# Kernel optimization log

Hardware: AMD Instinct MI355X
Metric: run time of the kernel (lower is better)

Reference implementation:

```python
import jax, jax.numpy as jnp
from jax import lax
import numpy as np

DIM = 384
NUM_HEADS = 8
HEAD_DIM = DIM // NUM_HEADS


def setup_inputs() -> dict:
    key = jax.random.key(0)
    k_x, k_qw, k_qb, k_lw, k_lb = jax.random.split(key, 5)
    B, H, W = 2, 64, 64
    N = H * W
    x = jax.random.normal(k_x, (B, N, DIM), dtype=jnp.float32)
    # nn.Linear(dim, 3*dim): weight (3C, C), bias (3C,)
    qkv_w = jax.random.normal(k_qw, (3 * DIM, DIM), dtype=jnp.float32) * (1.0 / np.sqrt(DIM))
    qkv_b = jax.random.normal(k_qb, (3 * DIM,), dtype=jnp.float32) * 0.02
    # nn.Conv2d(dim, dim, 3, padding=1, groups=dim): weight (C, 1, 3, 3), bias (C,)
    lepe_w = jax.random.normal(k_lw, (DIM, 1, 3, 3), dtype=jnp.float32) * (1.0 / 3.0)
    lepe_b = jax.random.normal(k_lb, (DIM,), dtype=jnp.float32) * 0.02
    return {"x": x, "qkv_w": qkv_w, "qkv_b": qkv_b, "lepe_w": lepe_w, "lepe_b": lepe_b, "H": H, "W": W}


def reference(x, qkv_w, qkv_b, lepe_w, lepe_b, H, W):
    B, N, C = x.shape
    hd = C // NUM_HEADS
    scale = hd ** -0.5
    # qkv projection: (B, N, 3C) -> (B, N, 3, heads, head_dim)
    qkv = (jnp.einsum('bnc,oc->bno', x, qkv_w) + qkv_b).reshape(B, N, 3, NUM_HEADS, hd)
    q, k, v = qkv[:, :, 0], qkv[:, :, 1], qkv[:, :, 2]  # each (B, N, heads, hd)
    attn = jnp.einsum('bnhd,bmhd->bhnm', q * scale, k)   # (B, heads, N, N)
    attn = jax.nn.softmax(attn, axis=-1)
    out = jnp.einsum('bhnm,bmhd->bnhd', attn, v).reshape(B, N, C)
    # LePE: depthwise 3x3 conv on v in NCHW layout
    v_img = v.reshape(B, H, W, C).transpose(0, 3, 1, 2)  # (B, C, H, W)
    lepe = lax.conv_general_dilated(
        v_img, lepe_w, window_strides=(1, 1), padding='SAME',
        feature_group_count=C,
        dimension_numbers=('NCHW', 'OIHW', 'NCHW'))
    lepe = lepe + lepe_b[None, :, None, None]
    return out + lepe.transpose(0, 2, 3, 1).reshape(B, N, C)
```

## Files before the change

kernel.cpp:

```cpp
#include <hip/hip_runtime.h>
#include <stdint.h>

#define DIM   384
#define NH    8
#define HD    48
#define HDP   64
#define NTOK  4096
#define KDIM  384
#define SCALE 0.14433756729740643f

typedef float  f32x4   __attribute__((ext_vector_type(4)));
typedef float  f32x16  __attribute__((ext_vector_type(16)));
typedef __bf16 bf16x8  __attribute__((ext_vector_type(8)));

__device__ __forceinline__ unsigned short f2bf(float f) {
  union { float f; unsigned int u; } c; c.f = f;
  unsigned int r = (c.u + 0x7FFFu + ((c.u >> 16) & 1u)) >> 16;
  return (unsigned short)r;
}
__device__ __forceinline__ float bf2f(unsigned short h) {
  union { unsigned int u; float f; } c; c.u = ((unsigned int)h) << 16;
  return c.f;
}


__global__ void prep_kernel(const float* __restrict__ x, const float* __restrict__ w,
                            unsigned short* __restrict__ x_bf,
                            unsigned short* __restrict__ w_bf) {
  int tid = blockIdx.x * blockDim.x + threadIdx.x;
  int stride = gridDim.x * blockDim.x;
  for (int i = tid; i < 786432; i += stride) {
    float4 v = ((const float4*)x)[i];
    ushort4 o;
    o.x = f2bf(v.x); o.y = f2bf(v.y); o.z = f2bf(v.z); o.w = f2bf(v.w);
    ((ushort4*)x_bf)[i] = o;
  }
  for (int i = tid; i < 110592; i += stride) {
    float4 v = ((const float4*)w)[i];
    ushort4 o;
    o.x = f2bf(v.x); o.y = f2bf(v.y); o.z = f2bf(v.z); o.w = f2bf(v.w);
    ((ushort4*)w_bf)[i] = o;
  }
}

__global__ __launch_bounds__(256) void qkv_gemm(
    const unsigned short* __restrict__ A,
    const unsigned short* __restrict__ Bw,
    const float* __restrict__ bias,
    unsigned short* __restrict__ q_pad,
    unsigned short* __restrict__ k_pad,
    unsigned short* __restrict__ v_t) {
  __shared__ unsigned short ldsA[128 * 32];
  __shared__ unsigned short ldsB[64 * 32];
  const int tid = threadIdx.x;
  const int wv = tid >> 6, ln = tid & 63;
  const int lrow = ln & 15, lq = ln >> 4;
  const int m0 = blockIdx.x * 128;
  const int n0 = blockIdx.y * 64;
  const int wm = (wv >> 1) * 64, wn = (wv & 1) * 32;

  f32x4 acc[4][2];
#pragma unroll
  for (int mi = 0; mi < 4; ++mi)
#pragma unroll
    for (int ni = 0; ni < 2; ++ni)
#pragma unroll
      for (int r = 0; r < 4; ++r) acc[mi][ni][r] = 0.f;

  for (int k0 = 0; k0 < KDIM; k0 += 32) {
    __syncthreads();
#pragma unroll
    for (int j = 0; j < 2; ++j) {
      int r16 = wv * 2 + j;
      const unsigned short* ga = A + (size_t)(m0 + r16 * 16 + (ln >> 2)) * KDIM
                                   + k0 + (ln & 3) * 8;
      __builtin_amdgcn_global_load_lds(
          (const __attribute__((address_space(1))) void*)ga,
          (__attribute__((address_space(3))) void*)&ldsA[r16 * 512], 16, 0, 0);
    }
    const unsigned short* gb = Bw + (size_t)(n0 + wv * 16 + (ln >> 2)) * KDIM
                                  + k0 + (ln & 3) * 8;
    __builtin_amdgcn_global_load_lds(
        (const __attribute__((address_space(1))) void*)gb,
        (__attribute__((address_space(3))) void*)&ldsB[wv * 512], 16, 0, 0);
    __syncthreads();
    bf16x8 af[4], bfv[2];
#pragma unroll
    for (int mi = 0; mi < 4; ++mi)
      af[mi] = *(const bf16x8*)&ldsA[(wm + mi * 16 + lrow) * 32 + lq * 8];
#pragma unroll
    for (int ni = 0; ni < 2; ++ni)
      bfv[ni] = *(const bf16x8*)&ldsB[(wn + ni * 16 + lrow) * 32 + lq * 8];
#pragma unroll
    for (int mi = 0; mi < 4; ++mi)
#pragma unroll
      for (int ni = 0; ni < 2; ++ni)
        acc[mi][ni] = __builtin_amdgcn_mfma_f32_16x16x32_bf16(
            af[mi], bfv[ni], acc[mi][ni], 0, 0, 0);
  }

#pragma unroll
  for (int mi = 0; mi < 4; ++mi)
#pragma unroll
    for (int ni = 0; ni < 2; ++ni)
#pragma unroll
      for (int r = 0; r < 4; ++r) {
        int row = m0 + wm + mi * 16 + lq * 4 + r;
        int col = n0 + wn + ni * 16 + lrow;
        float val = acc[mi][ni][r] + bias[col];
        int b = row >> 12;
        int n = row & 4095;
        if (col < 384) {
          int h = col / 48, d = col - h * 48;
          q_pad[((size_t)(b * 8 + h) * NTOK + n) * HDP + d] = f2bf(val * SCALE);
        } else if (col < 768) {
          int o = col - 384;
          int h = o / 48, d = o - h * 48;
          k_pad[((size_t)(b * 8 + h) * NTOK + n) * HDP + d] = f2bf(val);
        } else {
          int o = col - 768;
          v_t[((size_t)b * DIM + o) * NTOK + n] = f2bf(val);
        }
      }
}

__global__ __launch_bounds__(256) void lepe_kernel(
    const unsigned short* __restrict__ v_t,
    const float* __restrict__ lw, const float* __restrict__ lb,
    float* __restrict__ out) {
  __shared__ __align__(16) unsigned short pl[16 * 648];
  const int cg = blockIdx.x;
  const int sy = blockIdx.y;
  const int b  = blockIdx.z;
  const int t = threadIdx.x;
  const int y0 = sy * 8;
#pragma unroll
  for (int i = 0; i < 5; ++i) {
    int id = t + i * 256;
    int c = id / 80, rem = id - c * 80;
    int row = rem >> 3, cx = rem & 7;
    int y = y0 - 1 + row;
    uint4 val = make_uint4(0u, 0u, 0u, 0u);
    if (y >= 0 && y < 64)
      val = *(const uint4*)(v_t + ((size_t)(b * DIM + cg * 16 + c)) * NTOK + y * 64 + cx * 8);
    *(uint4*)&pl[c * 648 + row * 64 + cx * 8] = val;
  }
  __syncthreads();
  const int c = t & 15, pg = t >> 4;
  const int cglob = cg * 16 + c;
  float w[9];
#pragma unroll
  for (int j = 0; j < 9; ++j) w[j] = lw[cglob * 9 + j];
  const float bias = lb[cglob];
  const unsigned short* base = &pl[c * 648];
  for (int i = 0; i < 32; ++i) {
    int p = pg * 32 + i;
    int lr = p >> 6, x = p & 63;
    float acc = bias;
#pragma unroll
    for (int ky = 0; ky < 3; ++ky)
#pragma unroll
      for (int kx = 0; kx < 3; ++kx) {
        int xx = x + kx - 1;
        if (xx >= 0 && xx < 64)
          acc += w[ky * 3 + kx] * bf2f(base[(lr + ky) * 64 + xx]);
      }
    out[((size_t)(b * NTOK + sy * 512 + p)) * DIM + cglob] = acc;
  }
}

__global__ __launch_bounds__(256, 4) void attn_kernel(
    const unsigned short* __restrict__ q_pad,
    const unsigned short* __restrict__ k_pad,
    const unsigned short* __restrict__ v_t,
    float* __restrict__ out) {
  __shared__ __align__(16) char smem[31232];
  unsigned short* Kl = (unsigned short*)smem;
  unsigned short* Vl = (unsigned short*)(smem + 16384);
  float* Lsum = (float*)(smem + 28672);
  float* Ol   = (float*)smem;

  const int tid = threadIdx.x;
  const int wv = tid >> 6, ln = tid & 63;
  const int kh = wv >> 1;
  const int wq = wv & 1;
  const int l31 = ln & 31, hh = ln >> 5;
  const int th = tid & 127;
  const int qb = blockIdx.x, bh = blockIdx.y;
  const int b = bh >> 3, hd = bh & 7;

  const int qrb_self = wq * 32 + l31;
  const unsigned short* qp = q_pad + ((size_t)bh * NTOK + qb * 64 + qrb_self) * HDP + hh * 8;
  bf16x8 Qf[4];
#pragma unroll
  for (int hs = 0; hs < 4; ++hs)
    Qf[hs] = *(const bf16x8*)(qp + hs * 16);

  f32x16 Oacc[2];
#pragma unroll
  for (int dc = 0; dc < 2; ++dc)
#pragma unroll
    for (int r = 0; r < 16; ++r) Oacc[dc][r] = 0.f;
  float lsum = 0.f;

  const unsigned short* kbase = k_pad + (size_t)bh * NTOK * HDP;
  const unsigned short* vbase = v_t + ((size_t)b * DIM + hd * HD) * NTOK;
  unsigned short* Kh = Kl + kh * 4096;
  unsigned short* Vh = Vl + kh * 3072;

  for (int it = 0; it < 32; ++it) {
    const int kt = kh * 32 + it;
    __syncthreads();
    const unsigned short* kg = kbase + (size_t)kt * 64 * HDP;
#pragma unroll
    for (int i = 0; i < 4; ++i) {
      int idx = th + i * 128;
      int r = idx >> 3, cc = idx & 7;
      uint4 val = *(const uint4*)(kg + r * HDP + cc * 8);
      *(uint4*)&Kh[r * 64 + ((cc ^ (r & 7)) * 8)] = val;
    }
    const unsigned short* vg = vbase + kt * 64;
#pragma unroll
    for (int i = 0; i < 3; ++i) {
      int idx = th + i * 128;
      int d = idx >> 3, cc = idx & 7;
      uint4 val = *(const uint4*)(vg + (size_t)d * NTOK + cc * 8);
      *(uint4*)&Vh[d * 64 + ((cc ^ (d & 7)) * 8)] = val;
    }
    __syncthreads();

    unsigned int P32[16];
#pragma unroll
    for (int C = 0; C < 2; ++C) {
      f32x16 s;
#pragma unroll
      for (int r = 0; r < 16; ++r) s[r] = 0.f;
      const int krow = C * 32 + l31;
#pragma unroll
      for (int hs = 0; hs < 4; ++hs) {
        bf16x8 kf = *(const bf16x8*)&Kh[krow * 64 + (((hs * 2 + hh) ^ (krow & 7)) * 8)];
        s = __builtin_amdgcn_mfma_f32_32x32x16_bf16(kf, Qf[hs], s, 0, 0, 0);
      }
#pragma unroll
      for (int t8 = 0; t8 < 8; ++t8) {
        float e0 = __expf(s[2 * t8]);
        float e1 = __expf(s[2 * t8 + 1]);
        lsum += e0 + e1;
        P32[C * 8 + t8] = __builtin_amdgcn_perm(
            __float_as_uint(e1), __float_as_uint(e0), 0x07060302u);
      }
    }

#pragma unroll
    for (int s4 = 0; s4 < 4; ++s4) {
      const int o = (s4 >> 1) * 8 + (s4 & 1) * 4;
      unsigned int x0 = (unsigned int)__shfl_xor((int)P32[o + 0], 32, 64);
      unsigned int x1 = (unsigned int)__shfl_xor((int)P32[o + 1], 32, 64);
      unsigned int x2 = (unsigned int)__shfl_xor((int)P32[o + 2], 32, 64);
      unsigned int x3 = (unsigned int)__shfl_xor((int)P32[o + 3], 32, 64);
      union { unsigned int u[4]; bf16x8 v; } pa;
      pa.u[0] = hh ? x2 : P32[o + 0];
      pa.u[1] = hh ? x3 : P32[o + 1];
      pa.u[2] = hh ? P32[o + 2] : x0;
      pa.u[3] = hh ? P32[o + 3] : x1;
#pragma unroll
      for (int dc = 0; dc < 2; ++dc) {
        int vrow = dc * 32 + l31;
        bf16x8 vf = *(const bf16x8*)&Vh[vrow * 64 + (((s4 * 2 + hh) ^ (vrow & 7)) * 8)];
        Oacc[dc] = __builtin_amdgcn_mfma_f32_32x32x16_bf16(pa.v, vf, Oacc[dc], 0, 0, 0);
      }
    }
  }

  lsum += __shfl_xor(lsum, 32, 64);
  __syncthreads();
  if (kh == 1) {
#pragma unroll
    for (int dc = 0; dc < 2; ++dc)
#pragma unroll
      for (int r = 0; r < 16; ++r) {
        int qrb = wq * 32 + (r & 3) + 8 * (r >> 2) + 4 * hh;
        int d = dc * 32 + l31;
        if (d < HD) Ol[qrb * HD + d] = Oacc[dc][r];
      }
    if (hh == 0) Lsum[64 + wq * 32 + l31] = lsum;
  } else {
    if (hh == 0) Lsum[wq * 32 + l31] = lsum;
  }
  __syncthreads();
  if (kh == 0) {
#pragma unroll
    for (int r = 0; r < 16; ++r) {
      int qrb = wq * 32 + (r & 3) + 8 * (r >> 2) + 4 * hh;
      float lt = Lsum[qrb] + Lsum[64 + qrb];
      float linv = 1.0f / lt;
      float* op = out + ((size_t)(b * NTOK + qb * 64 + qrb)) * DIM + hd * HD;
#pragma unroll
      for (int dc = 0; dc < 2; ++dc) {
        int d = dc * 32 + l31;
        if (d < HD) op[d] += (Oacc[dc][r] + Ol[qrb * HD + d]) * linv;
      }
    }
  }
}

extern "C" void kernel_launch(void* const* d_in, const int* in_sizes, int n_in,
                              void* d_out, int out_size, void* d_ws, size_t ws_size,
                              hipStream_t stream) {
  const float* x      = (const float*)d_in[0];
  const float* qkv_w  = (const float*)d_in[1];
  const float* qkv_b  = (const float*)d_in[2];
  const float* lepe_w = (const float*)d_in[3];
  const float* lepe_b = (const float*)d_in[4];

  char* ws = (char*)d_ws;
  unsigned short* x_bf  = (unsigned short*)(ws);
  unsigned short* w_bf  = (unsigned short*)(ws + 6291456);
  unsigned short* q_pad = (unsigned short*)(ws + 7176192);
  unsigned short* k_pad = (unsigned short*)(ws + 15564800);
  unsigned short* v_t   = (unsigned short*)(ws + 23953408);
  float* out = (float*)d_out;

  hipMemsetAsync(q_pad, 0, 8388608, stream);
  prep_kernel<<<1024, 256, 0, stream>>>(x, qkv_w, x_bf, w_bf);
  qkv_gemm<<<dim3(64, 18), 256, 0, stream>>>(x_bf, w_bf, qkv_b, q_pad, k_pad, v_t);
  lepe_kernel<<<dim3(24, 8, 2), 256, 0, stream>>>(v_t, lepe_w, lepe_b, out);
  attn_kernel<<<dim3(64, 16), 256, 0, stream>>>(q_pad, k_pad, v_t, out);
}
```

Measured before the change: 222.8 us.

## Drop head-dim padding, use exp2 and ones-row trick for softmax sums

Stores Q and K compactly with head dim 48 instead of padding to 64, which removes the memset and cuts the QK MFMAs from 4 to 3 per chunk, and stores K in LDS with a 56-element row stride. Folds log2(e) into the Q scale so exp2 can be used. It also writes a row of bf16 ones into the padded V rows so the PV MFMA yields the row sums, removing the scalar lsum accumulation. The cross-lane P exchange is halved to two shuffles. The risk is that the sums are now computed from bf16-rounded probabilities, and the 56-element K stride may cause LDS bank conflicts.

```diff
diff --git a/kernel.cpp b/kernel.cpp
--- a/kernel.cpp
+++ b/kernel.cpp
@@ -4,14 +4,19 @@
 #define DIM   384
 #define NH    8
 #define HD    48
-#define HDP   64
 #define NTOK  4096
 #define KDIM  384
-#define SCALE 0.14433756729740643f
+#define SCALEL2E 0.20823509610f
 
 typedef float  f32x4   __attribute__((ext_vector_type(4)));
 typedef float  f32x16  __attribute__((ext_vector_type(16)));
 typedef __bf16 bf16x8  __attribute__((ext_vector_type(8)));
+
+#if __has_builtin(__builtin_amdgcn_exp2f)
+#define EXP2F(x) __builtin_amdgcn_exp2f(x)
+#else
+#define EXP2F(x) exp2f(x)
+#endif
 
 __device__ __forceinline__ unsigned short f2bf(float f) {
   union { float f; unsigned int u; } c; c.f = f;
@@ -47,8 +52,8 @@
     const unsigned short* __restrict__ A,
     const unsigned short* __restrict__ Bw,
     const float* __restrict__ bias,
-    unsigned short* __restrict__ q_pad,
-    unsigned short* __restrict__ k_pad,
+    unsigned short* __restrict__ qc,
+    unsigned short* __restrict__ kc,
     unsigned short* __restrict__ v_t) {
   __shared__ unsigned short ldsA[128 * 32];
   __shared__ unsigned short ldsB[64 * 32];
@@ -112,11 +117,11 @@
         int n = row & 4095;
         if (col < 384) {
           int h = col / 48, d = col - h * 48;
-          q_pad[((size_t)(b * 8 + h) * NTOK + n) * HDP + d] = f2bf(val * SCALE);
+          qc[((size_t)(b * 8 + h) * NTOK + n) * HD + d] = f2bf(val * SCALEL2E);
         } else if (col < 768) {
           int o = col - 384;
           int h = o / 48, d = o - h * 48;
-          k_pad[((size_t)(b * 8 + h) * NTOK + n) * HDP + d] = f2bf(val);
+          kc[((size_t)(b * 8 + h) * NTOK + n) * HD + d] = f2bf(val);
         } else {
           int o = col - 768;
           v_t[((size_t)b * DIM + o) * NTOK + n] = f2bf(val);
@@ -170,14 +175,14 @@
 }
 
 __global__ __launch_bounds__(256, 4) void attn_kernel(
-    const unsigned short* __restrict__ q_pad,
-    const unsigned short* __restrict__ k_pad,
+    const unsigned short* __restrict__ qc,
+    const unsigned short* __restrict__ kcg,
     const unsigned short* __restrict__ v_t,
     float* __restrict__ out) {
   __shared__ __align__(16) char smem[31232];
   unsigned short* Kl = (unsigned short*)smem;
-  unsigned short* Vl = (unsigned short*)(smem + 16384);
-  float* Lsum = (float*)(smem + 28672);
+  unsigned short* Vl = (unsigned short*)(smem + 14336);
+  float* Lsum = (float*)(smem + 30720);
   float* Ol   = (float*)smem;
 
   const int tid = threadIdx.x;
@@ -189,11 +194,31 @@
   const int qb = blockIdx.x, bh = blockIdx.y;
   const int b = bh >> 3, hd = bh & 7;
 
+  unsigned short* Kh = Kl + kh * 3584;
+  unsigned short* Vh = Vl + kh * 4096;
+
+  int kro[3], kgo[3], vro[3], vgo[3];
+#pragma unroll
+  for (int i = 0; i < 3; ++i) {
+    int idx = th + i * 128;
+    int r = idx / 6, cc = idx - r * 6;
+    kro[i] = r * 56 + cc * 8;
+    kgo[i] = r * 48 + cc * 8;
+    int vd = idx >> 3, vc = idx & 7;
+    vro[i] = vd * 64 + ((vc ^ (vd & 7)) * 8);
+    vgo[i] = vd * 4096 + vc * 8;
+  }
+
+  if (th < 8) {
+    uint4 one4 = make_uint4(0x3F803F80u, 0x3F803F80u, 0x3F803F80u, 0x3F803F80u);
+    *(uint4*)&Vh[3072 + th * 8] = one4;
+  }
+
   const int qrb_self = wq * 32 + l31;
-  const unsigned short* qp = q_pad + ((size_t)bh * NTOK + qb * 64 + qrb_self) * HDP + hh * 8;
-  bf16x8 Qf[4];
-#pragma unroll
-  for (int hs = 0; hs < 4; ++hs)
+  const unsigned short* qp = qc + ((size_t)bh * NTOK + qb * 64 + qrb_self) * HD + hh * 8;
+  bf16x8 Qf[3];
+#pragma unroll
+  for (int hs = 0; hs < 3; ++hs)
     Qf[hs] = *(const bf16x8*)(qp + hs * 16);
 
   f32x16 Oacc[2];
@@ -201,31 +226,19 @@
   for (int dc = 0; dc < 2; ++dc)
 #pragma unroll
     for (int r = 0; r < 16; ++r) Oacc[dc][r] = 0.f;
-  float lsum = 0.f;
-
-  const unsigned short* kbase = k_pad + (size_t)bh * NTOK * HDP;
+
+  const unsigned short* kbase = kcg + (size_t)bh * NTOK * HD;
   const unsigned short* vbase = v_t + ((size_t)b * DIM + hd * HD) * NTOK;
-  unsigned short* Kh = Kl + kh * 4096;
-  unsigned short* Vh = Vl + kh * 3072;
 
   for (int it = 0; it < 32; ++it) {
     const int kt = kh * 32 + it;
     __syncthreads();
-    const unsigned short* kg = kbase + (size_t)kt * 64 * HDP;
-#pragma unroll
-    for (int i = 0; i < 4; ++i) {
-      int idx = th + i * 128;
-      int r = idx >> 3, cc = idx & 7;
-      uint4 val = *(const uint4*)(kg + r * HDP + cc * 8);
-      *(uint4*)&Kh[r * 64 + ((cc ^ (r & 7)) * 8)] = val;
-    }
+    const unsigned short* kg = kbase + (size_t)kt * 64 * HD;
     const unsigned short* vg = vbase + kt * 64;
 #pragma unroll
     for (int i = 0; i < 3; ++i) {
-      int idx = th + i * 128;
-      int d = idx >> 3, cc = idx & 7;
-      uint4 val = *(const uint4*)(vg + (size_t)d * NTOK + cc * 8);
-      *(uint4*)&Vh[d * 64 + ((cc ^ (d & 7)) * 8)] = val;
+      *(uint4*)&Kh[kro[i]] = *(const uint4*)(kg + kgo[i]);
+      *(uint4*)&Vh[vro[i]] = *(const uint4*)(vg + vgo[i]);
     }
     __syncthreads();
 
@@ -235,17 +248,16 @@
       f32x16 s;
 #pragma unroll
       for (int r = 0; r < 16; ++r) s[r] = 0.f;
-      const int krow = C * 32 + l31;
-#pragma unroll
-      for (int hs = 0; hs < 4; ++hs) {
-        bf16x8 kf = *(const bf16x8*)&Kh[krow * 64 + (((hs * 2 + hh) ^ (krow & 7)) * 8)];
+      const unsigned short* kr = &Kh[(C * 32 + l31) * 56 + hh * 8];
+#pragma unroll
+      for (int hs = 0; hs < 3; ++hs) {
+        bf16x8 kf = *(const bf16x8*)(kr + hs * 16);
         s = __builtin_amdgcn_mfma_f32_32x32x16_bf16(kf, Qf[hs], s, 0, 0, 0);
       }
 #pragma unroll
       for (int t8 = 0; t8 < 8; ++t8) {
-        float e0 = __expf(s[2 * t8]);
-        float e1 = __expf(s[2 * t8 + 1]);
-        lsum += e0 + e1;
+        float e0 = EXP2F(s[2 * t8]);
+        float e1 = EXP2F(s[2 * t8 + 1]);
         P32[C * 8 + t8] = __builtin_amdgcn_perm(
             __float_as_uint(e1), __float_as_uint(e0), 0x07060302u);
       }
@@ -254,15 +266,15 @@
 #pragma unroll
     for (int s4 = 0; s4 < 4; ++s4) {
       const int o = (s4 >> 1) * 8 + (s4 & 1) * 4;
-      unsigned int x0 = (unsigned int)__shfl_xor((int)P32[o + 0], 32, 64);
-      unsigned int x1 = (unsigned int)__shfl_xor((int)P32[o + 1], 32, 64);
-      unsigned int x2 = (unsigned int)__shfl_xor((int)P32[o + 2], 32, 64);
-      unsigned int x3 = (unsigned int)__shfl_xor((int)P32[o + 3], 32, 64);
+      unsigned int send1 = hh ? P32[o + 0] : P32[o + 2];
+      unsigned int send2 = hh ? P32[o + 1] : P32[o + 3];
+      unsigned int recv1 = (unsigned int)__shfl_xor((int)send1, 32, 64);
+      unsigned int recv2 = (unsigned int)__shfl_xor((int)send2, 32, 64);
       union { unsigned int u[4]; bf16x8 v; } pa;
-      pa.u[0] = hh ? x2 : P32[o + 0];
-      pa.u[1] = hh ? x3 : P32[o + 1];
-      pa.u[2] = hh ? P32[o + 2] : x0;
-      pa.u[3] = hh ? P32[o + 3] : x1;
+      pa.u[0] = hh ? recv1 : P32[o + 0];
+      pa.u[1] = hh ? recv2 : P32[o + 1];
+      pa.u[2] = hh ? P32[o + 2] : recv1;
+      pa.u[3] = hh ? P32[o + 3] : recv2;
 #pragma unroll
       for (int dc = 0; dc < 2; ++dc) {
         int vrow = dc * 32 + l31;
@@ -272,34 +284,31 @@
     }
   }
 
-  lsum += __shfl_xor(lsum, 32, 64);
   __syncthreads();
+  if (l31 == 16) {
+#pragma unroll
+    for (int r = 0; r < 16; ++r) {
+      int qrb = wq * 32 + (r & 3) + 8 * (r >> 2) + 4 * hh;
+      Lsum[kh * 64 + qrb] = Oacc[1][r];
+    }
+  }
   if (kh == 1) {
 #pragma unroll
-    for (int dc = 0; dc < 2; ++dc)
-#pragma unroll
-      for (int r = 0; r < 16; ++r) {
-        int qrb = wq * 32 + (r & 3) + 8 * (r >> 2) + 4 * hh;
-        int d = dc * 32 + l31;
-        if (d < HD) Ol[qrb * HD + d] = Oacc[dc][r];
-      }
-    if (hh == 0) Lsum[64 + wq * 32 + l31] = lsum;
-  } else {
-    if (hh == 0) Lsum[wq * 32 + l31] = lsum;
+    for (int r = 0; r < 16; ++r) {
+      int qrb = wq * 32 + (r & 3) + 8 * (r >> 2) + 4 * hh;
+      Ol[qrb * 48 + l31] = Oacc[0][r];
+      if (l31 < 16) Ol[qrb * 48 + 32 + l31] = Oacc[1][r];
+    }
   }
   __syncthreads();
   if (kh == 0) {
 #pragma unroll
     for (int r = 0; r < 16; ++r) {
       int qrb = wq * 32 + (r & 3) + 8 * (r >> 2) + 4 * hh;
-      float lt = Lsum[qrb] + Lsum[64 + qrb];
-      float linv = 1.0f / lt;
+      float linv = 1.0f / (Lsum[qrb] + Lsum[64 + qrb]);
       float* op = out + ((size_t)(b * NTOK + qb * 64 + qrb)) * DIM + hd * HD;
-#pragma unroll
-      for (int dc = 0; dc < 2; ++dc) {
-        int d = dc * 32 + l31;
-        if (d < HD) op[d] += (Oacc[dc][r] + Ol[qrb * HD + d]) * linv;
-      }
+      op[l31] += (Oacc[0][r] + Ol[qrb * 48 + l31]) * linv;
+      if (l31 < 16) op[32 + l31] += (Oacc[1][r] + Ol[qrb * 48 + 32 + l31]) * linv;
     }
   }
 }
@@ -314,16 +323,15 @@
   const float* lepe_b = (const float*)d_in[4];
 
   char* ws = (char*)d_ws;
-  unsigned short* x_bf  = (unsigned short*)(ws);
-  unsigned short* w_bf  = (unsigned short*)(ws + 6291456);
-  unsigned short* q_pad = (unsigned short*)(ws + 7176192);
-  unsigned short* k_pad = (unsigned short*)(ws + 15564800);
-  unsigned short* v_t   = (unsigned short*)(ws + 23953408);
+  unsigned short* x_bf = (unsigned short*)(ws);
+  unsigned short* w_bf = (unsigned short*)(ws + 6291456);
+  unsigned short* qcp  = (unsigned short*)(ws + 7176192);
+  unsigned short* kcp  = (unsigned short*)(ws + 13467648);
+  unsigned short* v_t  = (unsigned short*)(ws + 19759104);
   float* out = (float*)d_out;
 
-  hipMemsetAsync(q_pad, 0, 8388608, stream);
   prep_kernel<<<1024, 256, 0, stream>>>(x, qkv_w, x_bf, w_bf);
-  qkv_gemm<<<dim3(64, 18), 256, 0, stream>>>(x_bf, w_bf, qkv_b, q_pad, k_pad, v_t);
+  qkv_gemm<<<dim3(64, 18), 256, 0, stream>>>(x_bf, w_bf, qkv_b, qcp, kcp, v_t);
   lepe_kernel<<<dim3(24, 8, 2), 256, 0, stream>>>(v_t, lepe_w, lepe_b, out);
-  attn_kernel<<<dim3(64, 16), 256, 0, stream>>>(q_pad, k_pad, v_t, out);
-}
+  attn_kernel<<<dim3(64, 16), 256, 0, stream>>>(qcp, kcp, v_t, out);
+}
```

Result: faster. 198.4 us (-11.0%).
